# Kernel optimization log

Measured on AMD Instinct MI355X. Metric: run time of the kernel, lower is better.

## Reference

```python
import jax, jax.numpy as jnp
import numpy as np

EMBED_DIM = 128
NUM_HEADS = 8
HEAD_DIM = EMBED_DIM // NUM_HEADS
SCALE = float(np.sqrt(HEAD_DIM))


def setup_inputs() -> dict:
    key = jax.random.key(0)
    ks = jax.random.split(key, 16)
    B, N, M, E = 16, 256, 256, EMBED_DIM
    s = 1.0 / np.sqrt(E)
    inp = {
        "query": jax.random.normal(ks[0], (B, N, E), jnp.float32),
        "key": jax.random.normal(ks[1], (B, M, E), jnp.float32),
        "value": jax.random.normal(ks[2], (B, M, E), jnp.float32),
        "rel_pe": jax.random.normal(ks[3], (B, N, M, E), jnp.float32),
        "attn_mask": jnp.zeros((B, N, M), jnp.float32),
        # linear params stored as [in, out]; y = x @ W + b
        "Wq": jax.random.normal(ks[4], (E, E), jnp.float32) * s,
        "bq": jnp.zeros((E,), jnp.float32),
        "Wk": jax.random.normal(ks[5], (E, E), jnp.float32) * s,
        "bk": jnp.zeros((E,), jnp.float32),
        "Wv": jax.random.normal(ks[6], (E, E), jnp.float32) * s,
        "bv": jnp.zeros((E,), jnp.float32),
        "Wpe": jax.random.normal(ks[7], (E, E), jnp.float32) * s,
        "bpe": jnp.zeros((E,), jnp.float32),
        "Wo": jax.random.normal(ks[8], (E, E), jnp.float32) * s,
        "bo": jnp.zeros((E,), jnp.float32),
    }
    return inp


def reference(query, key, value, rel_pe, attn_mask,
              Wq, bq, Wk, bk, Wv, bv, Wpe, bpe, Wo, bo):
    B, N, E = query.shape
    M = key.shape[1]
    H, D = NUM_HEADS, HEAD_DIM
    q = (query @ Wq + bq).reshape(B, N, H, D)
    k = (key @ Wk + bk).reshape(B, M, H, D)
    v = (value @ Wv + bv).reshape(B, M, H, D)
    pe = (rel_pe @ Wpe + bpe).reshape(B, N, M, H, D)
    score = jnp.einsum('bnhd,bmhd->bhnm', q, k) \
          + jnp.einsum('bnhd,bnmhd->bhnm', q, pe)
    score = score / SCALE + attn_mask[:, None, :, :]
    attn = jax.nn.softmax(score, axis=-1)
    attn = jnp.nan_to_num(attn, nan=0.0)  # dropout is identity in eval mode
    out = jnp.einsum('bhnm,bmhd->bnhd', attn, v) \
        + jnp.einsum('bhnm,bnmhd->bnhd', attn, pe)
    out = out.reshape(B, N, E)
    return out @ Wo + bo
```

## Files before the change

### kernel.cpp

```cpp
#include <hip/hip_runtime.h>
#include <hip/hip_bf16.h>
#include <math.h>

typedef __attribute__((ext_vector_type(8))) short bf16x8;
typedef __attribute__((ext_vector_type(4))) float f32x4;

__global__ void qkv_proj_kernel(const float* __restrict__ query,
                                const float* __restrict__ key,
                                const float* __restrict__ value,
                                const float* __restrict__ Wq, const float* __restrict__ bq,
                                const float* __restrict__ Wk, const float* __restrict__ bk,
                                const float* __restrict__ Wv, const float* __restrict__ bv,
                                float* __restrict__ qf, float* __restrict__ kf,
                                float* __restrict__ vf)
{
    const int mat = blockIdx.x >> 8;
    const int rb  = blockIdx.x & 255;
    const float* X; const float* W; const float* bias; float* dst;
    if (mat == 0)      { X = query; W = Wq; bias = bq; dst = qf; }
    else if (mat == 1) { X = key;   W = Wk; bias = bk; dst = kf; }
    else               { X = value; W = Wv; bias = bv; dst = vf; }

    __shared__ float sX[16][128];
    const int tid = threadIdx.x;
    const float* src = X + (size_t)rb * 16 * 128;
    #pragma unroll
    for (int i = 0; i < 8; ++i) {
        int idx = tid + i * 256;
        sX[idx >> 7][idx & 127] = src[idx];
    }
    __syncthreads();

    const int col = tid & 127;
    const int rg  = tid >> 7;
    float acc[8] = {0.f,0.f,0.f,0.f,0.f,0.f,0.f,0.f};
    for (int e = 0; e < 128; ++e) {
        float w = W[e * 128 + col];
        #pragma unroll
        for (int r = 0; r < 8; ++r) acc[r] += sX[rg * 8 + r][e] * w;
    }
    float bb = bias[col];
    #pragma unroll
    for (int r = 0; r < 8; ++r)
        dst[(size_t)(rb * 16 + rg * 8 + r) * 128 + col] = acc[r] + bb;
}

__global__ __launch_bounds__(256, 4) void mha_main_kernel(
    const float* __restrict__ relpe,
    const float* __restrict__ mask,
    const float* __restrict__ qf,
    const float* __restrict__ kf,
    const float* __restrict__ vf,
    const float* __restrict__ Wpe, const float* __restrict__ bpe,
    const float* __restrict__ Wo,  const float* __restrict__ bo,
    float* __restrict__ out)
{
    __shared__ __hip_bfloat16 sA[64][136];
    __shared__ __hip_bfloat16 sWt[16][136];
    __shared__ __hip_bfloat16 sPb[16][72];
    __shared__ float sS[8][256];
    __shared__ float sPf[8][64];
    __shared__ float sQs[128];
    __shared__ float sCb[8];
    __shared__ float sM[8], sL[8];
    __shared__ float sRf[16];
    __shared__ float sRed[128];
    __shared__ float sOut[128];

    const int tid  = threadIdx.x;
    const int lane = tid & 63;
    const int wv   = tid >> 6;
    const int bid  = ((blockIdx.x & 7) << 9) | (blockIdx.x >> 3);
    const int b    = bid >> 8;
    const int n    = bid & 255;
    const size_t bn = (size_t)(b * 256 + n);

    float4 pf[8];
    {
        const float4* s4 = (const float4*)(relpe + (bn * 256) * 128);
        #pragma unroll
        for (int i = 0; i < 8; ++i) pf[i] = s4[tid + i * 256];
    }

    if (tid < 128) sQs[tid] = qf[bn * 128 + tid] * 0.25f;
    if (tid < 8)  { sM[tid] = -INFINITY; sL[tid] = 0.f; }
    if (tid < 16) sRf[tid] = 1.f;
    if (tid < 72) {
        #pragma unroll
        for (int r = 8; r < 16; ++r) sPb[r][tid] = __float2bfloat16(0.f);
    }
    if (tid < 128) {
        #pragma unroll
        for (int r = 8; r < 16; ++r) sWt[r][tid] = __float2bfloat16(0.f);
    }
    __syncthreads();

    #pragma unroll
    for (int o = tid; o < 1024; o += 256) {
        int h = o >> 7, e = o & 127;
        const float4* wr = (const float4*)(Wpe + (size_t)e * 128 + h * 16);
        float4 w0 = wr[0], w1 = wr[1], w2 = wr[2], w3 = wr[3];
        const float* qh = &sQs[h * 16];
        float acc = w0.x*qh[0]+w0.y*qh[1]+w0.z*qh[2]+w0.w*qh[3]
                  + w1.x*qh[4]+w1.y*qh[5]+w1.z*qh[6]+w1.w*qh[7]
                  + w2.x*qh[8]+w2.y*qh[9]+w2.z*qh[10]+w2.w*qh[11]
                  + w3.x*qh[12]+w3.y*qh[13]+w3.z*qh[14]+w3.w*qh[15];
        sWt[h][e] = __float2bfloat16(acc);
    }
    if (tid < 8) {
        float acc = 0.f;
        #pragma unroll
        for (int d = 0; d < 16; ++d) acc += bpe[tid * 16 + d] * sQs[tid * 16 + d];
        sCb[tid] = acc;
    }

    const int hsc = tid >> 5;
    const int ml  = tid & 31;
    #pragma unroll
    for (int i = 0; i < 8; ++i) {
        int m = i * 32 + ml;
        const float4* k4 = (const float4*)(kf + ((size_t)(b * 256) + m) * 128 + hsc * 16);
        float4 ka = k4[0], kb = k4[1], kc = k4[2], kd = k4[3];
        const float* qh = &sQs[hsc * 16];
        float s = ka.x*qh[0]+ka.y*qh[1]+ka.z*qh[2]+ka.w*qh[3]
                + kb.x*qh[4]+kb.y*qh[5]+kb.z*qh[6]+kb.w*qh[7]
                + kc.x*qh[8]+kc.y*qh[9]+kc.z*qh[10]+kc.w*qh[11]
                + kd.x*qh[12]+kd.y*qh[13]+kd.z*qh[14]+kd.w*qh[15];
        sS[hsc][m] = s + mask[bn * 256 + m];
    }

    #pragma unroll
    for (int i = 0; i < 8; ++i) {
        int idx4 = tid + i * 256;
        int lr = idx4 >> 5, c4 = (idx4 & 31) * 4;
        __hip_bfloat162* dp = (__hip_bfloat162*)&sA[lr][c4];
        dp[0] = __float22bfloat162_rn(make_float2(pf[i].x, pf[i].y));
        dp[1] = __float22bfloat162_rn(make_float2(pf[i].z, pf[i].w));
    }
    __syncthreads();

    float out_acc = 0.f;
    f32x4 pr0 = {}, pr1 = {};
    const int e     = tid & 127;
    const int halfp = tid >> 7;
    const int hh    = e >> 4;
    const int arow  = lane & 15;
    const int koff  = lane >> 4;

    for (int t = 0; t < 4; ++t) {
        if (t < 3) {
            const float4* s4 = (const float4*)(relpe + (bn * 256 + (t + 1) * 64) * 128);
            #pragma unroll
            for (int i = 0; i < 8; ++i) pf[i] = s4[tid + i * 256];
        }

        f32x4 cs;
        #pragma unroll
        for (int r = 0; r < 4; ++r) {
            int row = wv * 16 + koff * 4 + r;
            cs[r] = (arow < 8) ? (sS[arow][t * 64 + row] + sCb[arow]) : 0.f;
        }
        #pragma unroll
        for (int kt = 0; kt < 4; ++kt) {
            bf16x8 af  = *(const bf16x8*)&sA[wv * 16 + arow][kt * 32 + koff * 8];
            bf16x8 bfr = *(const bf16x8*)&sWt[arow][kt * 32 + koff * 8];
            cs = __builtin_amdgcn_mfma_f32_16x16x32_bf16(af, bfr, cs, 0, 0, 0);
        }
        if (arow < 8) {
            #pragma unroll
            for (int r = 0; r < 4; ++r)
                sS[arow][t * 64 + wv * 16 + koff * 4 + r] = cs[r];
        }
        __syncthreads();

        {
            float sc0 = sS[hsc][t * 64 + ml];
            float sc1 = sS[hsc][t * 64 + ml + 32];
            float tm = fmaxf(sc0, sc1);
            #pragma unroll
            for (int m2 = 16; m2 >= 1; m2 >>= 1) tm = fmaxf(tm, __shfl_xor(tm, m2, 32));
            float mold = sM[hsc];
            float mnew = fmaxf(mold, tm);
            float p0 = __expf(sc0 - mnew), p1 = __expf(sc1 - mnew);
            float ts = p0 + p1;
            #pragma unroll
            for (int m2 = 16; m2 >= 1; m2 >>= 1) ts += __shfl_xor(ts, m2, 32);
            if (ml == 0) {
                float rf = __expf(mold - mnew);
                sRf[hsc] = rf;
                sM[hsc]  = mnew;
                sL[hsc]  = sL[hsc] * rf + ts;
            }
            sPf[hsc][ml]      = p0;
            sPf[hsc][ml + 32] = p1;
            sPb[hsc][ml]      = __float2bfloat16(p0);
            sPb[hsc][ml + 32] = __float2bfloat16(p1);
        }
        __syncthreads();

        {
            #pragma unroll
            for (int r = 0; r < 4; ++r) {
                float rf = sRf[koff * 4 + r];
                pr0[r] *= rf; pr1[r] *= rf;
            }
            #pragma unroll
            for (int kt = 0; kt < 2; ++kt) {
                bf16x8 ap = *(const bf16x8*)&sPb[arow][kt * 32 + koff * 8];
                bf16x8 b0, b1;
                #pragma unroll
                for (int j = 0; j < 8; ++j) {
                    int row = kt * 32 + koff * 8 + j;
                    b0[j] = *(const short*)&sA[row][wv * 32 + arow];
                    b1[j] = *(const short*)&sA[row][wv * 32 + 16 + arow];
                }
                pr0 = __builtin_amdgcn_mfma_f32_16x16x32_bf16(ap, b0, pr0, 0, 0, 0);
                pr1 = __builtin_amdgcn_mfma_f32_16x16x32_bf16(ap, b1, pr1, 0, 0, 0);
            }
            out_acc *= sRf[hh];
            const float* vp = vf + ((size_t)(b * 256) + t * 64 + halfp * 32) * 128 + e;
            const float* pp = &sPf[hh][halfp * 32];
            #pragma unroll 8
            for (int mm = 0; mm < 32; ++mm)
                out_acc += pp[mm] * vp[(size_t)mm * 128];
        }
        __syncthreads();

        if (t < 3) {
            #pragma unroll
            for (int i = 0; i < 8; ++i) {
                int idx4 = tid + i * 256;
                int lr = idx4 >> 5, c4 = (idx4 & 31) * 4;
                __hip_bfloat162* dp = (__hip_bfloat162*)&sA[lr][c4];
                dp[0] = __float22bfloat162_rn(make_float2(pf[i].x, pf[i].y));
                dp[1] = __float22bfloat162_rn(make_float2(pf[i].z, pf[i].w));
            }
            __syncthreads();
        }
    }

    if (halfp) sRed[e] = out_acc;
    #pragma unroll
    for (int r = 0; r < 4; ++r) {
        int row = koff * 4 + r;
        if (row < 8) {
            sS[row][wv * 32 + arow]      = pr0[r];
            sS[row][wv * 32 + 16 + arow] = pr1[r];
        }
    }
    __syncthreads();
    float outv = out_acc + (halfp ? 0.f : sRed[e]);
    __syncthreads();

    float ype = 0.f;
    {
        const float* wp  = Wpe + (size_t)(halfp * 64) * 128 + e;
        const float* prh = &sS[hh][halfp * 64];
        #pragma unroll 8
        for (int ee = 0; ee < 64; ++ee) ype += prh[ee] * wp[(size_t)ee * 128];
    }
    if (halfp) sRed[e] = ype;
    __syncthreads();
    if (!halfp) sOut[e] = (outv + ype + sRed[e]) / sL[hh] + bpe[e];
    __syncthreads();

    float y = 0.f;
    {
        const float* wo = Wo + (size_t)(halfp * 64) * 128 + e;
        #pragma unroll 8
        for (int ee = 0; ee < 64; ++ee) y += sOut[halfp * 64 + ee] * wo[(size_t)ee * 128];
    }
    if (halfp) sRed[e] = y;
    __syncthreads();
    if (!halfp) out[bn * 128 + e] = y + sRed[e] + bo[e];
}

extern "C" void kernel_launch(void* const* d_in, const int* in_sizes, int n_in,
                              void* d_out, int out_size, void* d_ws, size_t ws_size,
                              hipStream_t stream)
{
    const float* query = (const float*)d_in[0];
    const float* key   = (const float*)d_in[1];
    const float* value = (const float*)d_in[2];
    const float* relpe = (const float*)d_in[3];
    const float* mask  = (const float*)d_in[4];
    const float* Wq  = (const float*)d_in[5];
    const float* bq  = (const float*)d_in[6];
    const float* Wk  = (const float*)d_in[7];
    const float* bk  = (const float*)d_in[8];
    const float* Wv  = (const float*)d_in[9];
    const float* bv  = (const float*)d_in[10];
    const float* Wpe = (const float*)d_in[11];
    const float* bpe = (const float*)d_in[12];
    const float* Wo  = (const float*)d_in[13];
    const float* bo  = (const float*)d_in[14];
    float* out = (float*)d_out;

    float* qf = (float*)d_ws;
    float* kf = qf + 16 * 256 * 128;
    float* vf = kf + 16 * 256 * 128;

    qkv_proj_kernel<<<dim3(768), dim3(256), 0, stream>>>(
        query, key, value, Wq, bq, Wk, bk, Wv, bv, qf, kf, vf);
    mha_main_kernel<<<dim3(4096), dim3(256), 0, stream>>>(
        relpe, mask, qf, kf, vf, Wpe, bpe, Wo, bo, out);
}
```

Baseline: 219.4 us.

## Split key dimension across waves with per-wave online softmax and final merge

Each wave now owns a 64-key slice of the rel_pe rows and runs its own online softmax, score MFMAs and P·PE MFMAs on a private shared-memory region. This removes the block-wide barriers inside the key loop. The partial max, sum and accumulators are merged across waves at the end using an exp-rescaled reduction in shared memory. The change raises per-thread registers (16 float4 prefetch, 8 MFMA accumulators) and shared memory to about 58KB, and drops the occupancy hint from launch bounds, so fewer blocks may fit per CU.

```diff
diff --git a/kernel.cpp b/kernel.cpp
--- a/kernel.cpp
+++ b/kernel.cpp
@@ -45,7 +45,7 @@
         dst[(size_t)(rb * 16 + rg * 8 + r) * 128 + col] = acc[r] + bb;
 }
 
-__global__ __launch_bounds__(256, 4) void mha_main_kernel(
+__global__ __launch_bounds__(256) void mha_main_kernel(
     const float* __restrict__ relpe,
     const float* __restrict__ mask,
     const float* __restrict__ qf,
@@ -55,18 +55,7 @@
     const float* __restrict__ Wo,  const float* __restrict__ bo,
     float* __restrict__ out)
 {
-    __shared__ __hip_bfloat16 sA[64][136];
-    __shared__ __hip_bfloat16 sWt[16][136];
-    __shared__ __hip_bfloat16 sPb[16][72];
-    __shared__ float sS[8][256];
-    __shared__ float sPf[8][64];
-    __shared__ float sQs[128];
-    __shared__ float sCb[8];
-    __shared__ float sM[8], sL[8];
-    __shared__ float sRf[16];
-    __shared__ float sRed[128];
-    __shared__ float sOut[128];
-
+    __shared__ __align__(16) char smem[59424];
     const int tid  = threadIdx.x;
     const int lane = tid & 63;
     const int wv   = tid >> 6;
@@ -75,24 +64,19 @@
     const int n    = bid & 255;
     const size_t bn = (size_t)(b * 256 + n);
 
-    float4 pf[8];
-    {
-        const float4* s4 = (const float4*)(relpe + (bn * 256) * 128);
-        #pragma unroll
-        for (int i = 0; i < 8; ++i) pf[i] = s4[tid + i * 256];
-    }
+    char* wb = smem + wv * 13568;
+    __hip_bfloat16* sA  = (__hip_bfloat16*)wb;
+    float*          sQK = (float*)(wb + 8704);
+    __hip_bfloat16* sP  = (__hip_bfloat16*)(wb + 11008);
+    float*          sPf = (float*)(wb + 12288);
+    float*          sRf = (float*)(wb + 13440);
+    float*          sQs = (float*)(smem + 54272);
+    __hip_bfloat16* sWt = (__hip_bfloat16*)(smem + 54784);
+    float*          sCb = (float*)(smem + 59136);
+    float*          sMLm= (float*)(smem + 59168);
+    float*          sMLl= (float*)(smem + 59296);
 
     if (tid < 128) sQs[tid] = qf[bn * 128 + tid] * 0.25f;
-    if (tid < 8)  { sM[tid] = -INFINITY; sL[tid] = 0.f; }
-    if (tid < 16) sRf[tid] = 1.f;
-    if (tid < 72) {
-        #pragma unroll
-        for (int r = 8; r < 16; ++r) sPb[r][tid] = __float2bfloat16(0.f);
-    }
-    if (tid < 128) {
-        #pragma unroll
-        for (int r = 8; r < 16; ++r) sWt[r][tid] = __float2bfloat16(0.f);
-    }
     __syncthreads();
 
     #pragma unroll
@@ -100,12 +84,16 @@
         int h = o >> 7, e = o & 127;
         const float4* wr = (const float4*)(Wpe + (size_t)e * 128 + h * 16);
         float4 w0 = wr[0], w1 = wr[1], w2 = wr[2], w3 = wr[3];
-        const float* qh = &sQs[h * 16];
+        const float* qh = sQs + h * 16;
         float acc = w0.x*qh[0]+w0.y*qh[1]+w0.z*qh[2]+w0.w*qh[3]
                   + w1.x*qh[4]+w1.y*qh[5]+w1.z*qh[6]+w1.w*qh[7]
                   + w2.x*qh[8]+w2.y*qh[9]+w2.z*qh[10]+w2.w*qh[11]
                   + w3.x*qh[12]+w3.y*qh[13]+w3.z*qh[14]+w3.w*qh[15];
-        sWt[h][e] = __float2bfloat16(acc);
+        sWt[h * 136 + e] = __float2bfloat16(acc);
+    }
+    if (tid < 128) {
+        #pragma unroll
+        for (int r = 8; r < 16; ++r) sWt[r * 136 + tid] = __float2bfloat16(0.f);
     }
     if (tid < 8) {
         float acc = 0.f;
@@ -113,166 +101,206 @@
         for (int d = 0; d < 16; ++d) acc += bpe[tid * 16 + d] * sQs[tid * 16 + d];
         sCb[tid] = acc;
     }
-
-    const int hsc = tid >> 5;
-    const int ml  = tid & 31;
-    #pragma unroll
-    for (int i = 0; i < 8; ++i) {
-        int m = i * 32 + ml;
-        const float4* k4 = (const float4*)(kf + ((size_t)(b * 256) + m) * 128 + hsc * 16);
-        float4 ka = k4[0], kb = k4[1], kc = k4[2], kd = k4[3];
-        const float* qh = &sQs[hsc * 16];
-        float s = ka.x*qh[0]+ka.y*qh[1]+ka.z*qh[2]+ka.w*qh[3]
-                + kb.x*qh[4]+kb.y*qh[5]+kb.z*qh[6]+kb.w*qh[7]
-                + kc.x*qh[8]+kc.y*qh[9]+kc.z*qh[10]+kc.w*qh[11]
-                + kd.x*qh[12]+kd.y*qh[13]+kd.z*qh[14]+kd.w*qh[15];
-        sS[hsc][m] = s + mask[bn * 256 + m];
-    }
-
-    #pragma unroll
-    for (int i = 0; i < 8; ++i) {
-        int idx4 = tid + i * 256;
-        int lr = idx4 >> 5, c4 = (idx4 & 31) * 4;
-        __hip_bfloat162* dp = (__hip_bfloat162*)&sA[lr][c4];
-        dp[0] = __float22bfloat162_rn(make_float2(pf[i].x, pf[i].y));
-        dp[1] = __float22bfloat162_rn(make_float2(pf[i].z, pf[i].w));
-    }
-    __syncthreads();
-
-    float out_acc = 0.f;
-    f32x4 pr0 = {}, pr1 = {};
-    const int e     = tid & 127;
-    const int halfp = tid >> 7;
-    const int hh    = e >> 4;
-    const int arow  = lane & 15;
-    const int koff  = lane >> 4;
-
-    for (int t = 0; t < 4; ++t) {
-        if (t < 3) {
-            const float4* s4 = (const float4*)(relpe + (bn * 256 + (t + 1) * 64) * 128);
+    __syncthreads();
+
+    const int mw = wv * 64;
+
+    {
+        const int hq = lane & 7;
+        const int rg = lane >> 3;
+        float qreg[16];
+        #pragma unroll
+        for (int i = 0; i < 4; ++i)
+            ((float4*)qreg)[i] = ((const float4*)(sQs + hq * 16))[i];
+        float cb = sCb[hq];
+        #pragma unroll
+        for (int p = 0; p < 8; ++p) {
+            int row = p * 8 + rg;
+            const float4* kr = (const float4*)(kf + ((size_t)(b * 256) + mw + row) * 128 + hq * 16);
+            float4 k0 = kr[0], k1 = kr[1], k2 = kr[2], k3 = kr[3];
+            float s = k0.x*qreg[0]+k0.y*qreg[1]+k0.z*qreg[2]+k0.w*qreg[3]
+                    + k1.x*qreg[4]+k1.y*qreg[5]+k1.z*qreg[6]+k1.w*qreg[7]
+                    + k2.x*qreg[8]+k2.y*qreg[9]+k2.z*qreg[10]+k2.w*qreg[11]
+                    + k3.x*qreg[12]+k3.y*qreg[13]+k3.z*qreg[14]+k3.w*qreg[15];
+            sQK[row * 9 + hq] = s + cb + mask[bn * 256 + mw + row];
+        }
+    }
+
+    float4 pf[16];
+    {
+        const float4* rp = (const float4*)(relpe + (bn * 256 + mw) * 128);
+        #pragma unroll
+        for (int i = 0; i < 16; ++i) pf[i] = rp[i * 64 + lane];
+    }
+
+    const int arow = lane & 15;
+    const int koff = lane >> 4;
+    float m_run = -INFINITY, l_run = 0.f;
+    f32x4 pr[8] = {};
+    float oa0 = 0.f, oa1 = 0.f;
+
+    #pragma unroll
+    for (int st = 0; st < 2; ++st) {
+        #pragma unroll
+        for (int i = 0; i < 16; ++i) {
+            int row = 2 * i + (lane >> 5);
+            int col = (lane & 31) * 4;
+            union { __hip_bfloat162 h2[2]; uint2 u; } pk;
+            pk.h2[0] = __float22bfloat162_rn(make_float2(pf[i].x, pf[i].y));
+            pk.h2[1] = __float22bfloat162_rn(make_float2(pf[i].z, pf[i].w));
+            *(uint2*)&sA[row * 136 + col] = pk.u;
+        }
+        if (st == 0) {
+            const float4* rp = (const float4*)(relpe + (bn * 256 + mw + 32) * 128);
             #pragma unroll
-            for (int i = 0; i < 8; ++i) pf[i] = s4[tid + i * 256];
-        }
-
-        f32x4 cs;
+            for (int i = 0; i < 16; ++i) pf[i] = rp[i * 64 + lane];
+        }
+
+        f32x4 cs0, cs1;
         #pragma unroll
         for (int r = 0; r < 4; ++r) {
-            int row = wv * 16 + koff * 4 + r;
-            cs[r] = (arow < 8) ? (sS[arow][t * 64 + row] + sCb[arow]) : 0.f;
+            int rb0 = st * 32 + koff * 4 + r;
+            cs0[r] = (arow < 8) ? sQK[rb0 * 9 + arow] : 0.f;
+            cs1[r] = (arow < 8) ? sQK[(rb0 + 16) * 9 + arow] : 0.f;
         }
         #pragma unroll
         for (int kt = 0; kt < 4; ++kt) {
-            bf16x8 af  = *(const bf16x8*)&sA[wv * 16 + arow][kt * 32 + koff * 8];
-            bf16x8 bfr = *(const bf16x8*)&sWt[arow][kt * 32 + koff * 8];
-            cs = __builtin_amdgcn_mfma_f32_16x16x32_bf16(af, bfr, cs, 0, 0, 0);
-        }
-        if (arow < 8) {
+            bf16x8 bw = *(const bf16x8*)&sWt[arow * 136 + kt * 32 + koff * 8];
+            bf16x8 a0 = *(const bf16x8*)&sA[arow * 136 + kt * 32 + koff * 8];
+            bf16x8 a1 = *(const bf16x8*)&sA[(16 + arow) * 136 + kt * 32 + koff * 8];
+            cs0 = __builtin_amdgcn_mfma_f32_16x16x32_bf16(a0, bw, cs0, 0, 0, 0);
+            cs1 = __builtin_amdgcn_mfma_f32_16x16x32_bf16(a1, bw, cs1, 0, 0, 0);
+        }
+
+        float tm = fmaxf(fmaxf(fmaxf(cs0[0], cs0[1]), fmaxf(cs0[2], cs0[3])),
+                         fmaxf(fmaxf(cs1[0], cs1[1]), fmaxf(cs1[2], cs1[3])));
+        tm = fmaxf(tm, __shfl_xor(tm, 16));
+        tm = fmaxf(tm, __shfl_xor(tm, 32));
+        float mnew = fmaxf(m_run, tm);
+        float p0[4], p1[4]; float ts = 0.f;
+        #pragma unroll
+        for (int r = 0; r < 4; ++r) {
+            p0[r] = __expf(cs0[r] - mnew); ts += p0[r];
+            p1[r] = __expf(cs1[r] - mnew); ts += p1[r];
+        }
+        ts += __shfl_xor(ts, 16);
+        ts += __shfl_xor(ts, 32);
+        float rf = __expf(m_run - mnew);
+        l_run = l_run * rf + ts;
+        m_run = mnew;
+        if (koff == 0) sRf[arow] = rf;
+
+        #pragma unroll
+        for (int r = 0; r < 4; ++r) {
+            int ml0 = koff * 4 + r;
+            sP[arow * 40 + ml0]      = __float2bfloat16(p0[r]);
+            sP[arow * 40 + ml0 + 16] = __float2bfloat16(p1[r]);
+            if (arow < 8) {
+                sPf[ml0 * 9 + arow]        = p0[r];
+                sPf[(ml0 + 16) * 9 + arow] = p1[r];
+            }
+        }
+
+        float rfr[4];
+        #pragma unroll
+        for (int r = 0; r < 4; ++r) rfr[r] = sRf[koff * 4 + r];
+        #pragma unroll
+        for (int es = 0; es < 8; ++es) {
             #pragma unroll
-            for (int r = 0; r < 4; ++r)
-                sS[arow][t * 64 + wv * 16 + koff * 4 + r] = cs[r];
-        }
-        __syncthreads();
-
-        {
-            float sc0 = sS[hsc][t * 64 + ml];
-            float sc1 = sS[hsc][t * 64 + ml + 32];
-            float tm = fmaxf(sc0, sc1);
+            for (int r = 0; r < 4; ++r) pr[es][r] *= rfr[r];
+        }
+        float rpv = sRf[lane >> 3];
+        oa0 *= rpv; oa1 *= rpv;
+
+        bf16x8 ap = *(const bf16x8*)&sP[arow * 40 + koff * 8];
+        #pragma unroll
+        for (int es = 0; es < 8; ++es) {
+            bf16x8 bv;
             #pragma unroll
-            for (int m2 = 16; m2 >= 1; m2 >>= 1) tm = fmaxf(tm, __shfl_xor(tm, m2, 32));
-            float mold = sM[hsc];
-            float mnew = fmaxf(mold, tm);
-            float p0 = __expf(sc0 - mnew), p1 = __expf(sc1 - mnew);
-            float ts = p0 + p1;
+            for (int j = 0; j < 8; ++j)
+                bv[j] = *(const short*)&sA[(koff * 8 + j) * 136 + es * 16 + arow];
+            pr[es] = __builtin_amdgcn_mfma_f32_16x16x32_bf16(ap, bv, pr[es], 0, 0, 0);
+        }
+
+        const float* vp = vf + ((size_t)(b * 256) + mw + st * 32) * 128 + 2 * lane;
+        const int hpv = lane >> 3;
+        #pragma unroll
+        for (int mm = 0; mm < 32; ++mm) {
+            float2 v2 = *(const float2*)(vp + (size_t)mm * 128);
+            float pw = sPf[mm * 9 + hpv];
+            oa0 += pw * v2.x; oa1 += pw * v2.y;
+        }
+    }
+
+    if (koff == 0 && arow < 8) { sMLm[wv * 8 + arow] = m_run; sMLl[wv * 8 + arow] = l_run; }
+    __syncthreads();
+
+    float* sPrAcc = (float*)smem;
+    float* sOutAcc = (float*)(smem + 16384);
+    #pragma unroll
+    for (int r = 0; r < 4; ++r) {
+        int hrow = koff * 4 + r;
+        if (hrow < 8) {
+            float M = fmaxf(fmaxf(sMLm[hrow], sMLm[8 + hrow]),
+                            fmaxf(sMLm[16 + hrow], sMLm[24 + hrow]));
+            float sc = __expf(sMLm[wv * 8 + hrow] - M);
             #pragma unroll
-            for (int m2 = 16; m2 >= 1; m2 >>= 1) ts += __shfl_xor(ts, m2, 32);
-            if (ml == 0) {
-                float rf = __expf(mold - mnew);
-                sRf[hsc] = rf;
-                sM[hsc]  = mnew;
-                sL[hsc]  = sL[hsc] * rf + ts;
-            }
-            sPf[hsc][ml]      = p0;
-            sPf[hsc][ml + 32] = p1;
-            sPb[hsc][ml]      = __float2bfloat16(p0);
-            sPb[hsc][ml + 32] = __float2bfloat16(p1);
-        }
-        __syncthreads();
-
-        {
-            #pragma unroll
-            for (int r = 0; r < 4; ++r) {
-                float rf = sRf[koff * 4 + r];
-                pr0[r] *= rf; pr1[r] *= rf;
-            }
-            #pragma unroll
-            for (int kt = 0; kt < 2; ++kt) {
-                bf16x8 ap = *(const bf16x8*)&sPb[arow][kt * 32 + koff * 8];
-                bf16x8 b0, b1;
-                #pragma unroll
-                for (int j = 0; j < 8; ++j) {
-                    int row = kt * 32 + koff * 8 + j;
-                    b0[j] = *(const short*)&sA[row][wv * 32 + arow];
-                    b1[j] = *(const short*)&sA[row][wv * 32 + 16 + arow];
-                }
-                pr0 = __builtin_amdgcn_mfma_f32_16x16x32_bf16(ap, b0, pr0, 0, 0, 0);
-                pr1 = __builtin_amdgcn_mfma_f32_16x16x32_bf16(ap, b1, pr1, 0, 0, 0);
-            }
-            out_acc *= sRf[hh];
-            const float* vp = vf + ((size_t)(b * 256) + t * 64 + halfp * 32) * 128 + e;
-            const float* pp = &sPf[hh][halfp * 32];
-            #pragma unroll 8
-            for (int mm = 0; mm < 32; ++mm)
-                out_acc += pp[mm] * vp[(size_t)mm * 128];
-        }
-        __syncthreads();
-
-        if (t < 3) {
-            #pragma unroll
-            for (int i = 0; i < 8; ++i) {
-                int idx4 = tid + i * 256;
-                int lr = idx4 >> 5, c4 = (idx4 & 31) * 4;
-                __hip_bfloat162* dp = (__hip_bfloat162*)&sA[lr][c4];
-                dp[0] = __float22bfloat162_rn(make_float2(pf[i].x, pf[i].y));
-                dp[1] = __float22bfloat162_rn(make_float2(pf[i].z, pf[i].w));
-            }
-            __syncthreads();
-        }
-    }
-
-    if (halfp) sRed[e] = out_acc;
-    #pragma unroll
-    for (int r = 0; r < 4; ++r) {
-        int row = koff * 4 + r;
-        if (row < 8) {
-            sS[row][wv * 32 + arow]      = pr0[r];
-            sS[row][wv * 32 + 16 + arow] = pr1[r];
-        }
-    }
-    __syncthreads();
-    float outv = out_acc + (halfp ? 0.f : sRed[e]);
-    __syncthreads();
-
+            for (int es = 0; es < 8; ++es)
+                sPrAcc[(wv * 8 + hrow) * 128 + es * 16 + arow] = pr[es][r] * sc;
+        }
+    }
+    {
+        int hpv = lane >> 3;
+        float M = fmaxf(fmaxf(sMLm[hpv], sMLm[8 + hpv]),
+                        fmaxf(sMLm[16 + hpv], sMLm[24 + hpv]));
+        float sc = __expf(sMLm[wv * 8 + hpv] - M);
+        sOutAcc[wv * 128 + 2 * lane]     = oa0 * sc;
+        sOutAcc[wv * 128 + 2 * lane + 1] = oa1 * sc;
+    }
+    __syncthreads();
+
+    float* sPrS  = (float*)(smem + 18432);
+    float* sOutS = (float*)(smem + 22528);
+    #pragma unroll
+    for (int i = 0; i < 4; ++i) {
+        int idx = tid + 256 * i;
+        sPrS[idx] = sPrAcc[idx] + sPrAcc[1024 + idx] + sPrAcc[2048 + idx] + sPrAcc[3072 + idx];
+    }
+    if (tid < 128)
+        sOutS[tid] = sOutAcc[tid] + sOutAcc[128 + tid] + sOutAcc[256 + tid] + sOutAcc[384 + tid];
+    __syncthreads();
+
+    float* sRed  = (float*)(smem + 23040);
+    float* sOutF = (float*)(smem + 23552);
+    const int e = tid & 127, half = tid >> 7, hh = e >> 4;
     float ype = 0.f;
     {
-        const float* wp  = Wpe + (size_t)(halfp * 64) * 128 + e;
-        const float* prh = &sS[hh][halfp * 64];
+        const float* wp  = Wpe + (size_t)(half * 64) * 128 + e;
+        const float* prh = &sPrS[hh * 128 + half * 64];
         #pragma unroll 8
         for (int ee = 0; ee < 64; ++ee) ype += prh[ee] * wp[(size_t)ee * 128];
     }
-    if (halfp) sRed[e] = ype;
-    __syncthreads();
-    if (!halfp) sOut[e] = (outv + ype + sRed[e]) / sL[hh] + bpe[e];
+    if (half) sRed[e] = ype;
+    __syncthreads();
+    if (!half) {
+        float M = fmaxf(fmaxf(sMLm[hh], sMLm[8 + hh]), fmaxf(sMLm[16 + hh], sMLm[24 + hh]));
+        float L = sMLl[hh]      * __expf(sMLm[hh] - M)
+                + sMLl[8 + hh]  * __expf(sMLm[8 + hh] - M)
+                + sMLl[16 + hh] * __expf(sMLm[16 + hh] - M)
+                + sMLl[24 + hh] * __expf(sMLm[24 + hh] - M);
+        sOutF[e] = (sOutS[e] + ype + sRed[e]) / L + bpe[e];
+    }
     __syncthreads();
 
     float y = 0.f;
     {
-        const float* wo = Wo + (size_t)(halfp * 64) * 128 + e;
+        const float* wo = Wo + (size_t)(half * 64) * 128 + e;
         #pragma unroll 8
-        for (int ee = 0; ee < 64; ++ee) y += sOut[halfp * 64 + ee] * wo[(size_t)ee * 128];
-    }
-    if (halfp) sRed[e] = y;
-    __syncthreads();
-    if (!halfp) out[bn * 128 + e] = y + sRed[e] + bo[e];
+        for (int ee = 0; ee < 64; ++ee) y += sOutF[half * 64 + ee] * wo[(size_t)ee * 128];
+    }
+    if (half) sRed[e] = y;
+    __syncthreads();
+    if (!half) out[bn * 128 + e] = y + sRed[e] + bo[e];
 }
 
 extern "C" void kernel_launch(void* const* d_in, const int* in_sizes, int n_in,
```

After: 304.9 us. 1.39x slower.
